# Kernel optimization log

Hardware: AMD Instinct MI355X
Metric: run time of the kernel (lower is better)

Reference implementation:

```python
import jax, jax.numpy as jnp
import numpy as np

WINDOW = 5  # len_sort_window in the original module


def setup_inputs() -> dict:
    key = jax.random.key(0)
    k1, k2, k3 = jax.random.split(key, 3)
    B, L, D = 8, 4000, 512  # L divisible by WINDOW, D < L
    q = jax.random.normal(k1, (B, L, D), dtype=jnp.float32)
    k = jax.random.normal(k2, (B, L, D), dtype=jnp.float32)
    v = jax.random.normal(k3, (B, L, D), dtype=jnp.float32)
    return {"q": q, "k": k, "v": v}


def reference(q, k, v):
    # q, k are unused by the original forward.
    B, L, D = v.shape
    t = jnp.arange(L)          # sequence positions
    s = jnp.arange(D)          # per-feature cyclic shift amount (= feature index)
    # Shift feature i left by i: shifted[:, t, i] = v[:, (t + i) % L, i]
    idx_fwd = (t[:, None] + s[None, :]) % L            # [L, D]
    v_shift = jnp.take_along_axis(v, idx_fwd[None, :, :], axis=1)  # [B, L, D]
    # Sort within fixed non-overlapping windows of size WINDOW along the seq axis.
    v_sorted = jnp.sort(v_shift.reshape(B, L // WINDOW, WINDOW, D), axis=2)
    v_sorted = v_sorted.reshape(B, L, D)
    # Unshift feature i right by i: out[:, t, i] = v_sorted[:, (t - i) % L, i]
    idx_bwd = (t[:, None] - s[None, :]) % L            # [L, D]
    return jnp.take_along_axis(v_sorted, idx_bwd[None, :, :], axis=1)
```

## Files before the change

kernel.cpp:

```cpp
#include <hip/hip_runtime.h>


constexpr int L  = 4000;
constexpr int D  = 512;
constexpr int NG = L / 5;
constexpr int GCHUNK = NG / 8;

#define CE(a, b) { float lo_ = fminf(a, b); float hi_ = fmaxf(a, b); (a) = lo_; (b) = hi_; }

__global__ __launch_bounds__(256)
void swd18_col(const float* __restrict__ v, float* __restrict__ out) {
    const int lin  = blockIdx.x;
    const int xcd  = lin & 7;
    const int seq  = lin >> 3;
    const int b    = seq / (2 * GCHUNK);
    const int rest = seq % (2 * GCHUNK);
    const int gin  = rest >> 1;
    const int half = rest & 1;
    const int g    = xcd * GCHUNK + gin;

    const int i = half * 256 + threadIdx.x;

    const float* __restrict__ vb = v   + (size_t)b * (L * D);
    float*       __restrict__ ob = out + (size_t)b * (L * D);

    float r[15];
#pragma unroll
    for (int j = 0; j < 15; ++j) {
        int row = 5 * g - 5 + j;
        if (row < 0)  row += L;
        if (row >= L) row -= L;
        r[j] = vb[(size_t)row * D + i];
    }

    const int rc = i % 5;
    const bool e0 = rc == 0, e1 = rc == 1, e2 = rc == 2, e3 = rc == 3;

    float A0 = e0 ? r[0] : e1 ? r[1] : e2 ? r[2] : e3 ? r[3] : r[4];
    float A1 = e0 ? r[1] : e1 ? r[2] : e2 ? r[3] : e3 ? r[4] : r[5];
    float A2 = e0 ? r[2] : e1 ? r[3] : e2 ? r[4] : e3 ? r[5] : r[6];
    float A3 = e0 ? r[3] : e1 ? r[4] : e2 ? r[5] : e3 ? r[6] : r[7];
    float A4 = e0 ? r[4] : e1 ? r[5] : e2 ? r[6] : e3 ? r[7] : r[8];
    float B0 = e0 ? r[5] : e1 ? r[6] : e2 ? r[7] : e3 ? r[8] : r[9];
    float B1 = e0 ? r[6] : e1 ? r[7] : e2 ? r[8] : e3 ? r[9] : r[10];
    float B2 = e0 ? r[7] : e1 ? r[8] : e2 ? r[9] : e3 ? r[10] : r[11];
    float B3 = e0 ? r[8] : e1 ? r[9] : e2 ? r[10] : e3 ? r[11] : r[12];
    float B4 = e0 ? r[9] : e1 ? r[10] : e2 ? r[11] : e3 ? r[12] : r[13];

    CE(A0, A1) CE(A3, A4) CE(A2, A4) CE(A2, A3) CE(A1, A4)
    CE(A0, A3) CE(A0, A2) CE(A1, A3) CE(A1, A2)
    CE(B0, B1) CE(B3, B4) CE(B2, B4) CE(B2, B3) CE(B1, B4)
    CE(B0, B3) CE(B0, B2) CE(B1, B3) CE(B1, B2)

    float f0 = e0 ? B0 : e1 ? A4 : e2 ? A3 : e3 ? A2 : A1;
    float f1 = e0 ? B1 : e1 ? B0 : e2 ? A4 : e3 ? A3 : A2;
    float f2 = e0 ? B2 : e1 ? B1 : e2 ? B0 : e3 ? A4 : A3;
    float f3 = e0 ? B3 : e1 ? B2 : e2 ? B1 : e3 ? B0 : A4;
    float f4 = e0 ? B4 : e1 ? B3 : e2 ? B2 : e3 ? B1 : B0;

    float* o = ob + (size_t)(5 * g) * D + i;
    __builtin_nontemporal_store(f0, o + 0 * D);
    __builtin_nontemporal_store(f1, o + 1 * D);
    __builtin_nontemporal_store(f2, o + 2 * D);
    __builtin_nontemporal_store(f3, o + 3 * D);
    __builtin_nontemporal_store(f4, o + 4 * D);
}

#undef CE

extern "C" void kernel_launch(void* const* d_in, const int* in_sizes, int n_in,
                              void* d_out, int out_size, void* d_ws, size_t ws_size,
                              hipStream_t stream) {
    const float* v = (const float*)d_in[2];
    float* out = (float*)d_out;

    const int B = in_sizes[2] / (L * D);
    const int nblocks = B * NG * 2;
    swd18_col<<<dim3(nblocks), dim3(256), 0, stream>>>(v, out);
}
```

Before: 179.0 us.

## Process 20-row strips per block to cut halo re-reads

Each block now handles a 20-row strip (four 5-row output groups) instead of a single group, loading 30 rows instead of 15 per 5 output rows. This lowers redundant global reads of the overlapping halo rows from 3x to 1.5x and reduces the block count. It also drops the XCD-aware block swizzle in favour of a plain 2D grid, and raises register pressure with a 30-element register array, bounded by launch_bounds(256,6).

```diff
diff --git a/kernel.cpp b/kernel.cpp
--- a/kernel.cpp
+++ b/kernel.cpp
@@ -3,67 +3,76 @@
 
 constexpr int L  = 4000;
 constexpr int D  = 512;
-constexpr int NG = L / 5;
-constexpr int GCHUNK = NG / 8;
+constexpr int SROWS   = 20;
+constexpr int NSTRIPS = L / SROWS;
 
 #define CE(a, b) { float lo_ = fminf(a, b); float hi_ = fmaxf(a, b); (a) = lo_; (b) = hi_; }
 
-__global__ __launch_bounds__(256)
-void swd18_col(const float* __restrict__ v, float* __restrict__ out) {
-    const int lin  = blockIdx.x;
-    const int xcd  = lin & 7;
-    const int seq  = lin >> 3;
-    const int b    = seq / (2 * GCHUNK);
-    const int rest = seq % (2 * GCHUNK);
-    const int gin  = rest >> 1;
-    const int half = rest & 1;
-    const int g    = xcd * GCHUNK + gin;
-
-    const int i = half * 256 + threadIdx.x;
+__global__ __launch_bounds__(256, 6)
+void swd18_strip_scalar(const float* __restrict__ v, float* __restrict__ out) {
+    const int half  = blockIdx.x & 1;
+    const int strip = blockIdx.x >> 1;
+    const int b     = blockIdx.y;
+    const int i     = half * 256 + threadIdx.x;
 
     const float* __restrict__ vb = v   + (size_t)b * (L * D);
     float*       __restrict__ ob = out + (size_t)b * (L * D);
 
-    float r[15];
+    const int R0 = strip * SROWS;
+
+    float r[30];
+    {
+        int row = R0 - 5; if (row < 0) row += L;
 #pragma unroll
-    for (int j = 0; j < 15; ++j) {
-        int row = 5 * g - 5 + j;
-        if (row < 0)  row += L;
-        if (row >= L) row -= L;
-        r[j] = vb[(size_t)row * D + i];
+        for (int j = 0; j < 5; ++j)
+            r[j] = vb[(size_t)(row + j) * D + i];
+    }
+#pragma unroll
+    for (int j = 5; j < 25; ++j)
+        r[j] = vb[(size_t)(R0 + j - 5) * D + i];
+    {
+        int row = R0 + 20; if (row >= L) row -= L;
+#pragma unroll
+        for (int j = 25; j < 30; ++j)
+            r[j] = vb[(size_t)(row + j - 25) * D + i];
     }
 
     const int rc = i % 5;
     const bool e0 = rc == 0, e1 = rc == 1, e2 = rc == 2, e3 = rc == 3;
 
-    float A0 = e0 ? r[0] : e1 ? r[1] : e2 ? r[2] : e3 ? r[3] : r[4];
-    float A1 = e0 ? r[1] : e1 ? r[2] : e2 ? r[3] : e3 ? r[4] : r[5];
-    float A2 = e0 ? r[2] : e1 ? r[3] : e2 ? r[4] : e3 ? r[5] : r[6];
-    float A3 = e0 ? r[3] : e1 ? r[4] : e2 ? r[5] : e3 ? r[6] : r[7];
-    float A4 = e0 ? r[4] : e1 ? r[5] : e2 ? r[6] : e3 ? r[7] : r[8];
-    float B0 = e0 ? r[5] : e1 ? r[6] : e2 ? r[7] : e3 ? r[8] : r[9];
-    float B1 = e0 ? r[6] : e1 ? r[7] : e2 ? r[8] : e3 ? r[9] : r[10];
-    float B2 = e0 ? r[7] : e1 ? r[8] : e2 ? r[9] : e3 ? r[10] : r[11];
-    float B3 = e0 ? r[8] : e1 ? r[9] : e2 ? r[10] : e3 ? r[11] : r[12];
-    float B4 = e0 ? r[9] : e1 ? r[10] : e2 ? r[11] : e3 ? r[12] : r[13];
+#pragma unroll
+    for (int k = 0; k < 4; ++k) {
+        const float* p = &r[5 * k];
 
-    CE(A0, A1) CE(A3, A4) CE(A2, A4) CE(A2, A3) CE(A1, A4)
-    CE(A0, A3) CE(A0, A2) CE(A1, A3) CE(A1, A2)
-    CE(B0, B1) CE(B3, B4) CE(B2, B4) CE(B2, B3) CE(B1, B4)
-    CE(B0, B3) CE(B0, B2) CE(B1, B3) CE(B1, B2)
+        float A0 = e0 ? p[0] : e1 ? p[1] : e2 ? p[2] : e3 ? p[3] : p[4];
+        float A1 = e0 ? p[1] : e1 ? p[2] : e2 ? p[3] : e3 ? p[4] : p[5];
+        float A2 = e0 ? p[2] : e1 ? p[3] : e2 ? p[4] : e3 ? p[5] : p[6];
+        float A3 = e0 ? p[3] : e1 ? p[4] : e2 ? p[5] : e3 ? p[6] : p[7];
+        float A4 = e0 ? p[4] : e1 ? p[5] : e2 ? p[6] : e3 ? p[7] : p[8];
+        float B0 = e0 ? p[5] : e1 ? p[6] : e2 ? p[7] : e3 ? p[8] : p[9];
+        float B1 = e0 ? p[6] : e1 ? p[7] : e2 ? p[8] : e3 ? p[9] : p[10];
+        float B2 = e0 ? p[7] : e1 ? p[8] : e2 ? p[9] : e3 ? p[10] : p[11];
+        float B3 = e0 ? p[8] : e1 ? p[9] : e2 ? p[10] : e3 ? p[11] : p[12];
+        float B4 = e0 ? p[9] : e1 ? p[10] : e2 ? p[11] : e3 ? p[12] : p[13];
 
-    float f0 = e0 ? B0 : e1 ? A4 : e2 ? A3 : e3 ? A2 : A1;
-    float f1 = e0 ? B1 : e1 ? B0 : e2 ? A4 : e3 ? A3 : A2;
-    float f2 = e0 ? B2 : e1 ? B1 : e2 ? B0 : e3 ? A4 : A3;
-    float f3 = e0 ? B3 : e1 ? B2 : e2 ? B1 : e3 ? B0 : A4;
-    float f4 = e0 ? B4 : e1 ? B3 : e2 ? B2 : e3 ? B1 : B0;
+        CE(A0, A1) CE(A3, A4) CE(A2, A4) CE(A2, A3) CE(A1, A4)
+        CE(A0, A3) CE(A0, A2) CE(A1, A3) CE(A1, A2)
+        CE(B0, B1) CE(B3, B4) CE(B2, B4) CE(B2, B3) CE(B1, B4)
+        CE(B0, B3) CE(B0, B2) CE(B1, B3) CE(B1, B2)
 
-    float* o = ob + (size_t)(5 * g) * D + i;
-    __builtin_nontemporal_store(f0, o + 0 * D);
-    __builtin_nontemporal_store(f1, o + 1 * D);
-    __builtin_nontemporal_store(f2, o + 2 * D);
-    __builtin_nontemporal_store(f3, o + 3 * D);
-    __builtin_nontemporal_store(f4, o + 4 * D);
+        float f0 = e0 ? B0 : e1 ? A4 : e2 ? A3 : e3 ? A2 : A1;
+        float f1 = e0 ? B1 : e1 ? B0 : e2 ? A4 : e3 ? A3 : A2;
+        float f2 = e0 ? B2 : e1 ? B1 : e2 ? B0 : e3 ? A4 : A3;
+        float f3 = e0 ? B3 : e1 ? B2 : e2 ? B1 : e3 ? B0 : A4;
+        float f4 = e0 ? B4 : e1 ? B3 : e2 ? B2 : e3 ? B1 : B0;
+
+        float* o = ob + (size_t)(R0 + 5 * k) * D + i;
+        __builtin_nontemporal_store(f0, o + 0 * D);
+        __builtin_nontemporal_store(f1, o + 1 * D);
+        __builtin_nontemporal_store(f2, o + 2 * D);
+        __builtin_nontemporal_store(f3, o + 3 * D);
+        __builtin_nontemporal_store(f4, o + 4 * D);
+    }
 }
 
 #undef CE
@@ -75,6 +84,6 @@
     float* out = (float*)d_out;
 
     const int B = in_sizes[2] / (L * D);
-    const int nblocks = B * NG * 2;
-    swd18_col<<<dim3(nblocks), dim3(256), 0, stream>>>(v, out);
+    dim3 grid(NSTRIPS * 2, B);
+    swd18_strip_scalar<<<grid, dim3(256), 0, stream>>>(v, out);
 }
```

Result: no change. 176.6 us (-1.4%).
